# Kernel optimization log

Measured on AMD Instinct MI355X. Metric: run time of the kernel, lower is better.

Reference implementation:

```python
import jax, jax.numpy as jnp
import numpy as np

IN_C, OUT_C, K, STRIDE, PAD = 16, 32, 3, 1, 1


def setup_inputs() -> dict:
    key = jax.random.key(0)
    kx, kw = jax.random.split(key)
    x = jax.random.normal(kx, (2, IN_C, 8, 8, 32, 32), dtype=jnp.float32)
    # matches torch.randn init of nn.Parameter
    weight = jax.random.normal(kw, (OUT_C, IN_C, K, K, K, K), dtype=jnp.float32)
    bias = jnp.zeros((OUT_C,), dtype=jnp.float32)
    return {"x": x, "weight": weight, "bias": bias}


def _conv4d(x, weight):
    # 4 spatial dims; layout N C T D H W, weight O I kT kD kH kW.
    dn = jax.lax.ConvDimensionNumbers(
        lhs_spec=(0, 1, 2, 3, 4, 5),
        rhs_spec=(0, 1, 2, 3, 4, 5),
        out_spec=(0, 1, 2, 3, 4, 5),
    )
    return jax.lax.conv_general_dilated(
        x, weight,
        window_strides=(STRIDE,) * 4,
        padding=((PAD, PAD),) * 4,
        dimension_numbers=dn,
    )


def reference(x, weight, bias):
    # Same math as unfold(im2col) + matmul + bias in the torch module,
    # expressed as a single N-D convolution (implicit GEMM).
    out = _conv4d(x, weight)  # [B, out_c, oT, oD, oH, oW]
    return out + bias[None, :, None, None, None, None]
```

## Files before the change

### kernel.cpp

```cpp
#include <hip/hip_runtime.h>

#define IN_C  16
#define OUT_C 32
#define NB 2
#define TT 8
#define DD 8
#define HH 32
#define WW 32
#define TP 10
#define DP 10
#define HP 34
#define WPAD 34

#define XT_ROW_B  1088
#define XT_ELEMS  (NB*TP*DP*HP*2*WPAD*8)
#define WT_TAPS_P 84
#define WT_ELEMS  (WT_TAPS_P*2*OUT_C*8)

#define W_SLAB_B 5120

typedef __bf16 bf16x8 __attribute__((ext_vector_type(8)));
typedef float  f32x4  __attribute__((ext_vector_type(4)));
typedef float  f32x16 __attribute__((ext_vector_type(16)));

__device__ __forceinline__ unsigned short f2bf(float f) {
    unsigned int u = __builtin_bit_cast(unsigned int, f);
    u += 0x7fffu + ((u >> 16) & 1u);
    return (unsigned short)(u >> 16);
}

__device__ __forceinline__ void gload16(const void* g, void* l) {
    __builtin_amdgcn_global_load_lds(
        (const __attribute__((address_space(1))) unsigned int*)g,
        (__attribute__((address_space(3))) unsigned int*)l, 16, 0, 0);
}

__global__ __launch_bounds__(256) void prep_kernel(const float* __restrict__ x,
                                                   const float* __restrict__ wsrc,
                                                   unsigned short* __restrict__ xt,
                                                   unsigned short* __restrict__ wt) {
    int b = blockIdx.x;
    int tid = threadIdx.x;
    if (b < 4096) {
        __shared__ unsigned short ls[WW * IN_C];
        int h = b & 31, d = (b >> 5) & 7, t = (b >> 8) & 7, n = b >> 11;
        int c = tid >> 5, w = tid & 31;
        float v0 = x[((((size_t)(n * IN_C + c)     * TT + t) * DD + d) * HH + h) * WW + w];
        float v1 = x[((((size_t)(n * IN_C + c + 8) * TT + t) * DD + d) * HH + h) * WW + w];
        ls[w * 16 + c]     = f2bf(v0);
        ls[w * 16 + c + 8] = f2bf(v1);
        __syncthreads();
        if (tid < 68) {
            int blk = tid / 34, wl = tid % 34;
            unsigned char* row = (unsigned char*)xt +
                (size_t)(((n * TP + t + 1) * DP + d + 1) * HP + h + 1) * XT_ROW_B;
            f32x4 val = {0.f, 0.f, 0.f, 0.f};
            if (wl != 0 && wl != 33)
                val = *(const f32x4*)((const unsigned char*)ls + (wl - 1) * 32 + blk * 16);
            *(f32x4*)(row + tid * 16) = val;
        }
    } else if (b < 6800) {
        int j = b - 4096;
        int n, tp, dp, hp;
        if (j < 1360)      { n = j / 680;  int r = j % 680;  tp = (r / 340) * 9; int r2 = r % 340; dp = r2 / 34;       hp = r2 % 34; }
        else if (j < 2448) { int j2 = j - 1360; n = j2 / 544; int r = j2 % 544; tp = 1 + r / 68;  int r3 = r % 68;  dp = (r3 / 34) * 9; hp = r3 % 34; }
        else               { int j3 = j - 2448; n = j3 / 128; int r = j3 % 128; tp = 1 + r / 16;  int r4 = r % 16;  dp = 1 + r4 / 2;   hp = (r4 & 1) * 33; }
        if (tid < 68) {
            unsigned char* row = (unsigned char*)xt +
                (size_t)(((n * TP + tp) * DP + dp) * HP + hp) * XT_ROW_B;
            f32x4 z = {0.f, 0.f, 0.f, 0.f};
            *(f32x4*)(row + tid * 16) = z;
        }
    } else {
        int idx = (b - 6800) * 256 + tid;
        int tap = idx >> 9;
        int r = idx & 511;
        int icblk = r >> 8, oc = (r >> 3) & 31, i8 = r & 7;
        int ic = icblk * 8 + i8;
        float v = (tap < 81) ? wsrc[(oc * IN_C + ic) * 81 + tap] : 0.0f;
        wt[idx] = f2bf(v);
    }
}

__global__ __launch_bounds__(256, 2) void conv_main_kernel(const unsigned short* __restrict__ xt,
                                                           const unsigned short* __restrict__ wt,
                                                           const float* __restrict__ bias,
                                                           float* __restrict__ out) {
    __shared__ __align__(16) unsigned char As[4][2][W_SLAB_B];

    int bid = blockIdx.x;
    int lb  = (bid & 7) * 64 + (bid >> 3);
    int hb = lb & 3, d = (lb >> 2) & 7, t = (lb >> 5) & 7, n = lb >> 8;
    int h0 = hb * 8;
    int tid  = threadIdx.x;
    int wv   = tid >> 6;
    int lane = tid & 63;
    int l31  = lane & 31;
    int kblk = lane >> 5;

    int ab = kblk * 544 + l31 * 16;
    const unsigned char* wb = (const unsigned char*)wt + kblk * 512 + l31 * 16;
    const int rowbase = h0 + 2 * wv;

    auto asrc = [&](int p) {
        return (const unsigned char*)xt +
            (size_t)(((n * TP + t + p / 3) * DP + d + p % 3) * HP + rowbase) * XT_ROW_B;
    };

    unsigned char* slab0 = As[wv][0];
    unsigned char* slab1 = As[wv][1];

    {
        const unsigned char* s = asrc(0);
#pragma unroll
        for (int i = 0; i < 5; ++i)
            gload16(s + (lane + i * 64) * 16, slab0 + (lane + i * 64) * 16);
    }
    bf16x8 bf[2][9];
#pragma unroll
    for (int j = 0; j < 9; ++j)
        bf[0][j] = *(const bf16x8*)(wb + (size_t)j * 1024);

    f32x16 acc[2];
    acc[0] = {}; acc[1] = {};

#pragma unroll
    for (int p = 0; p < 9; ++p) {
        const int cur = p & 1, nxt = cur ^ 1;

        if (p < 8) {
            const unsigned char* s = asrc(p + 1);
            unsigned char* dstS = (p & 1) ? slab0 : slab1;
#pragma unroll
            for (int i = 0; i < 5; ++i)
                gload16(s + (lane + i * 64) * 16, dstS + (lane + i * 64) * 16);
            const unsigned char* bsrc = wb + (size_t)(p + 1) * 9216;
#pragma unroll
            for (int j = 0; j < 9; ++j)
                bf[nxt][j] = *(const bf16x8*)(bsrc + (size_t)j * 1024);
            asm volatile("s_waitcnt vmcnt(14)" ::: "memory");
        } else {
            asm volatile("s_waitcnt vmcnt(0)" ::: "memory");
        }
        __builtin_amdgcn_sched_barrier(0);

        const unsigned char* A = (p & 1) ? slab1 : slab0;
        bf16x8 a[12];
#pragma unroll
        for (int rr = 0; rr < 4; ++rr)
#pragma unroll
            for (int kw = 0; kw < 3; ++kw)
                a[rr * 3 + kw] = *(const bf16x8*)(A + rr * 1088 + ab + kw * 16);
        __builtin_amdgcn_sched_barrier(0);

        __builtin_amdgcn_s_setprio(1);
#pragma unroll
        for (int kw = 0; kw < 3; ++kw)
#pragma unroll
            for (int j = 0; j < 3; ++j) {
                acc[0] = __builtin_amdgcn_mfma_f32_32x32x16_bf16(a[j * 3 + kw],       bf[cur][j * 3 + kw], acc[0], 0, 0, 0);
                acc[1] = __builtin_amdgcn_mfma_f32_32x32x16_bf16(a[(j + 1) * 3 + kw], bf[cur][j * 3 + kw], acc[1], 0, 0, 0);
            }
        __builtin_amdgcn_s_setprio(0);
    }

    float bsv = bias[l31];
#pragma unroll
    for (int m = 0; m < 2; ++m) {
        int oh = h0 + 2 * wv + m;
        float* obase = out + (((((size_t)n * OUT_C + l31) * TT + t) * DD + d) * HH + oh) * WW;
#pragma unroll
        for (int q = 0; q < 4; ++q) {
            f32x4 v = { acc[m][4 * q + 0] + bsv, acc[m][4 * q + 1] + bsv,
                        acc[m][4 * q + 2] + bsv, acc[m][4 * q + 3] + bsv };
            *(f32x4*)(obase + 8 * q + 4 * kblk) = v;
        }
    }
}

extern "C" void kernel_launch(void* const* d_in, const int* in_sizes, int n_in,
                              void* d_out, int out_size, void* d_ws, size_t ws_size,
                              hipStream_t stream) {
    const float* x    = (const float*)d_in[0];
    const float* wsrc = (const float*)d_in[1];
    const float* bias = (const float*)d_in[2];
    float* out        = (float*)d_out;

    unsigned short* xt = (unsigned short*)d_ws;
    unsigned short* wt = xt + XT_ELEMS;

    prep_kernel<<<4096 + 2704 + 164, 256, 0, stream>>>(x, wsrc, xt, wt);
    conv_main_kernel<<<NB * TT * DD * 4, 256, 0, stream>>>(xt, wt, bias, out);
}
```

Baseline: 29.06 us.

## Drop LDS staging; load conv rows directly to registers with 4 rows per wave

Removes the LDS slabs and global_load_lds path. Each wave now loads its 6 padded input rows straight from global memory into registers, double-buffered by kT/kD position. Each of the 2 waves now computes 4 output rows instead of 2, so one weight fragment feeds four MFMAs, and the weights for a whole kT slice (27 taps) are held in registers. This is meant to remove LDS traffic and synchronization and to improve weight reuse. In exchange it raises register pressure considerably (two 18-entry A buffers, 27 B fragments, 4 accumulators), halves the threads per block, and depends on the hand-written vmcnt counts being correct.

Result: slower. 34.77 us (+19.6%).

```diff
diff --git a/kernel.cpp b/kernel.cpp
--- a/kernel.cpp
+++ b/kernel.cpp
@@ -17,8 +17,6 @@
 #define WT_TAPS_P 84
 #define WT_ELEMS  (WT_TAPS_P*2*OUT_C*8)
 
-#define W_SLAB_B 5120
-
 typedef __bf16 bf16x8 __attribute__((ext_vector_type(8)));
 typedef float  f32x4  __attribute__((ext_vector_type(4)));
 typedef float  f32x16 __attribute__((ext_vector_type(16)));
@@ -27,12 +25,6 @@
     unsigned int u = __builtin_bit_cast(unsigned int, f);
     u += 0x7fffu + ((u >> 16) & 1u);
     return (unsigned short)(u >> 16);
-}
-
-__device__ __forceinline__ void gload16(const void* g, void* l) {
-    __builtin_amdgcn_global_load_lds(
-        (const __attribute__((address_space(1))) unsigned int*)g,
-        (__attribute__((address_space(3))) unsigned int*)l, 16, 0, 0);
 }
 
 __global__ __launch_bounds__(256) void prep_kernel(const float* __restrict__ x,
@@ -82,12 +74,10 @@
     }
 }
 
-__global__ __launch_bounds__(256, 2) void conv_main_kernel(const unsigned short* __restrict__ xt,
-                                                           const unsigned short* __restrict__ wt,
-                                                           const float* __restrict__ bias,
-                                                           float* __restrict__ out) {
-    __shared__ __align__(16) unsigned char As[4][2][W_SLAB_B];
-
+__global__ __launch_bounds__(128) void conv_main_kernel(const unsigned short* __restrict__ xt,
+                                                        const unsigned short* __restrict__ wt,
+                                                        const float* __restrict__ bias,
+                                                        float* __restrict__ out) {
     int bid = blockIdx.x;
     int lb  = (bid & 7) * 64 + (bid >> 3);
     int hb = lb & 3, d = (lb >> 2) & 7, t = (lb >> 5) & 7, n = lb >> 8;
@@ -98,76 +88,66 @@
     int l31  = lane & 31;
     int kblk = lane >> 5;
 
-    int ab = kblk * 544 + l31 * 16;
-    const unsigned char* wb = (const unsigned char*)wt + kblk * 512 + l31 * 16;
-    const int rowbase = h0 + 2 * wv;
+    const int rowbase = h0 + 4 * wv;
 
-    auto asrc = [&](int p) {
-        return (const unsigned char*)xt +
-            (size_t)(((n * TP + t + p / 3) * DP + d + p % 3) * HP + rowbase) * XT_ROW_B;
+    bf16x8 a0[18], a1[18];
+    bf16x8 bq[27];
+    f32x16 acc[4];
+#pragma unroll
+    for (int m = 0; m < 4; ++m) acc[m] = {};
+
+    auto issueA = [&](int p, bf16x8 (&dst)[18]) {
+        const unsigned char* base = (const unsigned char*)xt +
+            (size_t)(((n * TP + t + p / 3) * DP + d + p % 3) * HP + rowbase) * XT_ROW_B +
+            kblk * 544 + l31 * 16;
+#pragma unroll
+        for (int r = 0; r < 6; ++r)
+#pragma unroll
+            for (int kw = 0; kw < 3; ++kw)
+                dst[r * 3 + kw] = *(const bf16x8*)(base + r * XT_ROW_B + kw * 16);
+    };
+    auto issueB = [&](int kt) {
+        const unsigned char* base = (const unsigned char*)wt +
+            (size_t)kt * 27 * 1024 + kblk * 512 + l31 * 16;
+#pragma unroll
+        for (int j = 0; j < 27; ++j)
+            bq[j] = *(const bf16x8*)(base + (size_t)j * 1024);
+    };
+    auto computeP = [&](const bf16x8 (&A)[18], int kd) {
+#pragma unroll
+        for (int kw = 0; kw < 3; ++kw)
+#pragma unroll
+            for (int kh = 0; kh < 3; ++kh)
+#pragma unroll
+                for (int m = 0; m < 4; ++m) {
+                    const int r = m + kh;
+                    acc[m] = __builtin_amdgcn_mfma_f32_32x32x16_bf16(
+                        A[r * 3 + kw], bq[kd * 9 + kh * 3 + kw], acc[m], 0, 0, 0);
+                }
     };
 
-    unsigned char* slab0 = As[wv][0];
-    unsigned char* slab1 = As[wv][1];
-
-    {
-        const unsigned char* s = asrc(0);
-#pragma unroll
-        for (int i = 0; i < 5; ++i)
-            gload16(s + (lane + i * 64) * 16, slab0 + (lane + i * 64) * 16);
-    }
-    bf16x8 bf[2][9];
-#pragma unroll
-    for (int j = 0; j < 9; ++j)
-        bf[0][j] = *(const bf16x8*)(wb + (size_t)j * 1024);
-
-    f32x16 acc[2];
-    acc[0] = {}; acc[1] = {};
+    issueA(0, a0);
+    issueB(0);
+    issueA(1, a1);
 
 #pragma unroll
     for (int p = 0; p < 9; ++p) {
-        const int cur = p & 1, nxt = cur ^ 1;
+        if (p < 8) asm volatile("s_waitcnt vmcnt(18)" ::: "memory");
+        else       asm volatile("s_waitcnt vmcnt(0)"  ::: "memory");
 
-        if (p < 8) {
-            const unsigned char* s = asrc(p + 1);
-            unsigned char* dstS = (p & 1) ? slab0 : slab1;
-#pragma unroll
-            for (int i = 0; i < 5; ++i)
-                gload16(s + (lane + i * 64) * 16, dstS + (lane + i * 64) * 16);
-            const unsigned char* bsrc = wb + (size_t)(p + 1) * 9216;
-#pragma unroll
-            for (int j = 0; j < 9; ++j)
-                bf[nxt][j] = *(const bf16x8*)(bsrc + (size_t)j * 1024);
-            asm volatile("s_waitcnt vmcnt(14)" ::: "memory");
-        } else {
-            asm volatile("s_waitcnt vmcnt(0)" ::: "memory");
+        if ((p & 1) == 0) computeP(a0, p % 3); else computeP(a1, p % 3);
+
+        if (p == 2) issueB(1);
+        if (p == 5) issueB(2);
+        if (p <= 6) {
+            if ((p & 1) == 0) issueA(p + 2, a0); else issueA(p + 2, a1);
         }
-        __builtin_amdgcn_sched_barrier(0);
-
-        const unsigned char* A = (p & 1) ? slab1 : slab0;
-        bf16x8 a[12];
-#pragma unroll
-        for (int rr = 0; rr < 4; ++rr)
-#pragma unroll
-            for (int kw = 0; kw < 3; ++kw)
-                a[rr * 3 + kw] = *(const bf16x8*)(A + rr * 1088 + ab + kw * 16);
-        __builtin_amdgcn_sched_barrier(0);
-
-        __builtin_amdgcn_s_setprio(1);
-#pragma unroll
-        for (int kw = 0; kw < 3; ++kw)
-#pragma unroll
-            for (int j = 0; j < 3; ++j) {
-                acc[0] = __builtin_amdgcn_mfma_f32_32x32x16_bf16(a[j * 3 + kw],       bf[cur][j * 3 + kw], acc[0], 0, 0, 0);
-                acc[1] = __builtin_amdgcn_mfma_f32_32x32x16_bf16(a[(j + 1) * 3 + kw], bf[cur][j * 3 + kw], acc[1], 0, 0, 0);
-            }
-        __builtin_amdgcn_s_setprio(0);
     }
 
     float bsv = bias[l31];
 #pragma unroll
-    for (int m = 0; m < 2; ++m) {
-        int oh = h0 + 2 * wv + m;
+    for (int m = 0; m < 4; ++m) {
+        int oh = rowbase + m;
         float* obase = out + (((((size_t)n * OUT_C + l31) * TT + t) * DD + d) * HH + oh) * WW;
 #pragma unroll
         for (int q = 0; q < 4; ++q) {
@@ -190,5 +170,5 @@
     unsigned short* wt = xt + XT_ELEMS;
 
     prep_kernel<<<4096 + 2704 + 164, 256, 0, stream>>>(x, wsrc, xt, wt);
-    conv_main_kernel<<<NB * TT * DD * 4, 256, 0, stream>>>(xt, wt, bias, out);
+    conv_main_kernel<<<NB * TT * DD * 4, 128, 0, stream>>>(xt, wt, bias, out);
 }
```
